# Performance work log

Hardware: AMD Instinct MI355X
Metric: run time of the kernel (lower is better)

The kernel has to match this reference:

```python
import jax, jax.numpy as jnp
import numpy as np

BETA = 0.01  # soft-threshold level (init kwarg)
EPS = 1e-12


def vector_to_toeplitz(v):
    # v: [2N-1] complex generator; T[i, j] = v[N-1 + i - j], shape [N, N]
    n = (v.shape[0] + 1) // 2
    ii = jnp.arange(n)[:, None]
    jj = jnp.arange(n)[None, :]
    return v[(n - 1) + ii - jj]


def soft_thresh(z, beta):
    # complex soft-threshold (proximal op of beta*||.||_1):
    # z * max(|z| - beta, 0) / |z|
    mag = jnp.abs(z)
    scale = jnp.maximum(mag - beta, 0.0) / jnp.maximum(mag, EPS)
    return z * scale.astype(z.real.dtype)


def setup_inputs() -> dict:
    key = jax.random.key(0)
    ks = jax.random.split(key, 8)
    N, M, B = 1024, 256, 1024
    d = jnp.float32
    return {
        "v_re": jax.random.normal(ks[0], (2 * N - 1,), d),
        "v_im": jax.random.normal(ks[1], (2 * N - 1,), d),
        "W2_re": jax.random.normal(ks[2], (N, M), d) / np.sqrt(M),
        "W2_im": jax.random.normal(ks[3], (N, M), d) / np.sqrt(M),
        "x_re": jax.random.normal(ks[4], (N, B), d),
        "x_im": jax.random.normal(ks[5], (N, B), d),
        "y_re": jax.random.normal(ks[6], (M, B), d),
        "y_im": jax.random.normal(ks[7], (M, B), d),
    }


def reference(v_re, v_im, W2_re, W2_im, x_re, x_im, y_re, y_im):
    v = jax.lax.complex(v_re, v_im)      # [2N-1]
    W2 = jax.lax.complex(W2_re, W2_im)   # [N, M] (= A^H)
    x = jax.lax.complex(x_re, x_im)      # [N, B]
    y = jax.lax.complex(y_re, y_im)      # [M, B]
    W1 = vector_to_toeplitz(v)           # [N, N] Toeplitz
    # tpm(W1, x) + W2 @ y, then complex soft-threshold
    z = soft_thresh(W1 @ x + W2 @ y, BETA)  # [N, B]
    return z
```

## Files before the change

kernel.cpp:

```cpp
#include <hip/hip_runtime.h>
#include <hip/hip_fp16.h>
#include <cstdint>
#include <cstddef>


#define K_DIM 2560
#define BETA_F 0.01f
#define EPS_F  1e-12f

typedef __attribute__((ext_vector_type(8))) _Float16 half8;
typedef __attribute__((ext_vector_type(4))) _Float16 half4;
typedef __attribute__((ext_vector_type(4))) float   floatx4;

__device__ alignas(16) _Float16 g_Ap[1024 * K_DIM];
__device__ alignas(16) _Float16 g_Bt[2048 * K_DIM];

__global__ __launch_bounds__(256) void build_all(
    const float* __restrict__ v_re, const float* __restrict__ v_im,
    const float* __restrict__ W2_re, const float* __restrict__ W2_im,
    const float* __restrict__ x_re, const float* __restrict__ x_im,
    const float* __restrict__ y_re, const float* __restrict__ y_im)
{
    const int bx = blockIdx.x;
    if (bx < 1280) {
        int t = bx * 256 + threadIdx.x;
        int i  = t / 320;
        int c  = t - i * 320;
        int kp = c * 8;
        half8 h;
        if (kp < 1024) {
#pragma unroll
            for (int j = 0; j < 8; ++j) h[j] = (_Float16)v_re[1023 + i - kp - j];
        } else if (kp < 1280) {
            const float* s = W2_re + i * 256 + (kp - 1024);
#pragma unroll
            for (int j = 0; j < 8; ++j) h[j] = (_Float16)s[j];
        } else if (kp < 2304) {
            int k2 = kp - 1280;
#pragma unroll
            for (int j = 0; j < 8; ++j) h[j] = (_Float16)v_im[1023 + i - k2 - j];
        } else {
            const float* s = W2_im + i * 256 + (kp - 2304);
#pragma unroll
            for (int j = 0; j < 8; ++j) h[j] = (_Float16)s[j];
        }
        *reinterpret_cast<half8*>(g_Ap + (size_t)i * K_DIM + kp) = h;
        return;
    }
    __shared__ float lre[32][33];
    __shared__ float lim[32][33];
    int idx = bx - 1280;
    int bk  = idx % 40;
    int by  = idx / 40;
    const float* sre = (bk < 32) ? x_re : y_re;
    const float* sim = (bk < 32) ? x_im : y_im;
    int kb   = (bk < 32) ? bk : (bk - 32);
    int koff = (bk < 32) ? 0 : 1024;
    int k0 = kb * 32;
    int n0 = by * 32;
    int tid = threadIdx.x;
    int tx = tid & 31, ty = tid >> 5;
#pragma unroll
    for (int s = 0; s < 4; ++s) {
        int kk = ty + 8 * s;
        lre[kk][tx] = sre[(size_t)(k0 + kk) * 1024 + n0 + tx];
        lim[kk][tx] = sim[(size_t)(k0 + kk) * 1024 + n0 + tx];
    }
    __syncthreads();
    int lane_n = tid >> 3;
    int kq     = (tid & 7) * 4;
    half4 hre, him, hmim;
#pragma unroll
    for (int j = 0; j < 4; ++j) {
        float re = lre[kq + j][lane_n];
        float im = lim[kq + j][lane_n];
        hre[j]  = (_Float16)re;
        him[j]  = (_Float16)im;
        hmim[j] = (_Float16)(-im);
    }
    int n = n0 + lane_n;
    size_t kk2 = (size_t)koff + k0 + kq;
    _Float16* r0 = g_Bt + (size_t)(2 * n)     * K_DIM;
    _Float16* r1 = g_Bt + (size_t)(2 * n + 1) * K_DIM;
    *reinterpret_cast<half4*>(r0 + kk2)        = hre;
    *reinterpret_cast<half4*>(r0 + kk2 + 1280) = hmim;
    *reinterpret_cast<half4*>(r1 + kk2)        = him;
    *reinterpret_cast<half4*>(r1 + kk2 + 1280) = hre;
}

__global__ __launch_bounds__(256, 2) void gemm_fused(float* __restrict__ out,
                                                     int out_n)
{
    __shared__ __align__(16) _Float16 As[2 * 4 * 64 * 32];
    __shared__ __align__(16) _Float16 Bs[2 * 4 * 64 * 32];

    const int tid  = threadIdx.x;
    const int lane = tid & 63;
    const int w    = tid >> 6;
    const int wm   = w >> 1;
    const int wn   = w & 1;

    const int bid = blockIdx.x;
    const int xcd = bid & 7;
    const int t   = bid >> 3;
    const int mi0 = ((xcd & 1) * 8 + (t & 7)) * 64;
    const int ni0 = ((xcd >> 1) * 8 + (t >> 3)) * 64;

    floatx4 acc[2][2];
#pragma unroll
    for (int a = 0; a < 2; ++a)
#pragma unroll
        for (int b = 0; b < 2; ++b) acc[a][b] = (floatx4)0.0f;

    const int rS = tid >> 2;
    const int jS = tid & 3;
    const int s0 = ((rS & 15) >> 1) & 3;
    char* asW = (char*)As + rS * 64 + ((jS ^ s0) * 16);
    char* bsW = (char*)Bs + rS * 64 + ((jS ^ s0) * 16);
    const _Float16* gA = g_Ap + (size_t)(mi0 + rS) * K_DIM + jS * 8;
    const _Float16* gB = g_Bt + (size_t)(ni0 + rS) * K_DIM + jS * 8;

    const int rowA = lane & 15;
    const int q    = lane >> 4;
    const int coff = (q ^ ((rowA >> 1) & 3)) * 16;

    const int NIT = K_DIM / 128;

    half8 sA[2][4], sB[2][4];

    {
        half8 tA[4], tB[4];
#pragma unroll
        for (int ks = 0; ks < 4; ++ks) {
            tA[ks] = *reinterpret_cast<const half8*>(gA + ks * 32);
            tB[ks] = *reinterpret_cast<const half8*>(gB + ks * 32);
        }
#pragma unroll
        for (int ks = 0; ks < 4; ++ks) {
            sA[1][ks] = *reinterpret_cast<const half8*>(gA + 128 + ks * 32);
            sB[1][ks] = *reinterpret_cast<const half8*>(gB + 128 + ks * 32);
        }
#pragma unroll
        for (int ks = 0; ks < 4; ++ks) {
            *reinterpret_cast<half8*>(asW + ks * 4096) = tA[ks];
            *reinterpret_cast<half8*>(bsW + ks * 4096) = tB[ks];
        }
    }
    __syncthreads();

#pragma unroll 2
    for (int kt = 0; kt < NIT; ++kt) {
        const int cur = kt & 1;
        const int nxt = cur ^ 1;
        if (kt + 2 < NIT) {
            const _Float16* ga = gA + (size_t)(kt + 2) * 128;
            const _Float16* gb = gB + (size_t)(kt + 2) * 128;
#pragma unroll
            for (int ks = 0; ks < 4; ++ks) {
                sA[cur][ks] = *reinterpret_cast<const half8*>(ga + ks * 32);
                sB[cur][ks] = *reinterpret_cast<const half8*>(gb + ks * 32);
            }
        }
        const char* Ab = (const char*)As + cur * 16384;
        const char* Bb = (const char*)Bs + cur * 16384;
#pragma unroll
        for (int ks = 0; ks < 4; ++ks) {
            half8 af[2], bf[2];
#pragma unroll
            for (int mi = 0; mi < 2; ++mi) {
                int r = wm * 32 + mi * 16 + rowA;
                af[mi] = *reinterpret_cast<const half8*>(Ab + ks * 4096 + r * 64 + coff);
            }
#pragma unroll
            for (int ni = 0; ni < 2; ++ni) {
                int r = wn * 32 + ni * 16 + rowA;
                bf[ni] = *reinterpret_cast<const half8*>(Bb + ks * 4096 + r * 64 + coff);
            }
#pragma unroll
            for (int mi = 0; mi < 2; ++mi)
#pragma unroll
                for (int ni = 0; ni < 2; ++ni)
                    acc[mi][ni] = __builtin_amdgcn_mfma_f32_16x16x32_f16(
                        af[mi], bf[ni], acc[mi][ni], 0, 0, 0);
        }
        if (kt + 1 < NIT) {
            char* aw = asW + nxt * 16384;
            char* bw = bsW + nxt * 16384;
#pragma unroll
            for (int ks = 0; ks < 4; ++ks) {
                *reinterpret_cast<half8*>(aw + ks * 4096) = sA[nxt][ks];
                *reinterpret_cast<half8*>(bw + ks * 4096) = sB[nxt][ks];
            }
        }
        __syncthreads();
    }

    const int colL  = lane & 15;
    const int rquad = (lane >> 4) * 4;
#pragma unroll
    for (int mi = 0; mi < 2; ++mi)
#pragma unroll
        for (int ni = 0; ni < 2; ++ni)
#pragma unroll
            for (int r = 0; r < 4; ++r) {
                float c = acc[mi][ni][r];
                float p = __shfl_xor(c, 1, 64);
                float mag = sqrtf(c * c + p * p);
                float s = fmaxf(mag - BETA_F, 0.0f) / fmaxf(mag, EPS_F);
                int row = mi0 + wm * 32 + mi * 16 + rquad + r;
                int col = ni0 + wn * 32 + ni * 16 + colL;
                if ((col & 1) == 0) {
                    size_t idx = (size_t)row * 1024 + (col >> 1);
                    if (idx < (size_t)out_n) out[idx] = c * s;
                }
            }
}

extern "C" void kernel_launch(void* const* d_in, const int* in_sizes, int n_in,
                              void* d_out, int out_size, void* d_ws, size_t ws_size,
                              hipStream_t stream) {
    (void)d_ws; (void)ws_size; (void)in_sizes; (void)n_in;
    const float* v_re  = (const float*)d_in[0];
    const float* v_im  = (const float*)d_in[1];
    const float* W2_re = (const float*)d_in[2];
    const float* W2_im = (const float*)d_in[3];
    const float* x_re  = (const float*)d_in[4];
    const float* x_im  = (const float*)d_in[5];
    const float* y_re  = (const float*)d_in[6];
    const float* y_im  = (const float*)d_in[7];
    float* out = (float*)d_out;

    build_all<<<2560, 256, 0, stream>>>(v_re, v_im, W2_re, W2_im,
                                        x_re, x_im, y_re, y_im);
    gemm_fused<<<512, 256, 0, stream>>>(out, out_size);
}
```

Baseline: 107.3 us.

## Merge pack and GEMM kernels into one cooperative kernel with grid sync

Merges the fp16 packing kernel and the fused GEMM+soft-threshold kernel into a single cooperative launch of 512 blocks. Each block packs five virtual pack blocks, then all blocks meet at a grid-wide barrier before the GEMM phase. The aim is to remove the second launch and the gap between the two kernels. In exchange it adds grid-sync overhead, needs all 512 blocks to be co-resident, and the pack phase now runs on fewer blocks and shares the GEMM kernel's resource limits.

```diff
diff --git a/kernel.cpp b/kernel.cpp
--- a/kernel.cpp
+++ b/kernel.cpp
@@ -1,5 +1,6 @@
 #include <hip/hip_runtime.h>
 #include <hip/hip_fp16.h>
+#include <hip/hip_cooperative_groups.h>
 #include <cstdint>
 #include <cstddef>
 
@@ -15,92 +16,96 @@
 __device__ alignas(16) _Float16 g_Ap[1024 * K_DIM];
 __device__ alignas(16) _Float16 g_Bt[2048 * K_DIM];
 
-__global__ __launch_bounds__(256) void build_all(
+namespace cg = cooperative_groups;
+
+__global__ __launch_bounds__(256, 2) void mega(
     const float* __restrict__ v_re, const float* __restrict__ v_im,
     const float* __restrict__ W2_re, const float* __restrict__ W2_im,
     const float* __restrict__ x_re, const float* __restrict__ x_im,
-    const float* __restrict__ y_re, const float* __restrict__ y_im)
-{
-    const int bx = blockIdx.x;
-    if (bx < 1280) {
-        int t = bx * 256 + threadIdx.x;
-        int i  = t / 320;
-        int c  = t - i * 320;
-        int kp = c * 8;
-        half8 h;
-        if (kp < 1024) {
-#pragma unroll
-            for (int j = 0; j < 8; ++j) h[j] = (_Float16)v_re[1023 + i - kp - j];
-        } else if (kp < 1280) {
-            const float* s = W2_re + i * 256 + (kp - 1024);
-#pragma unroll
-            for (int j = 0; j < 8; ++j) h[j] = (_Float16)s[j];
-        } else if (kp < 2304) {
-            int k2 = kp - 1280;
-#pragma unroll
-            for (int j = 0; j < 8; ++j) h[j] = (_Float16)v_im[1023 + i - k2 - j];
-        } else {
-            const float* s = W2_im + i * 256 + (kp - 2304);
-#pragma unroll
-            for (int j = 0; j < 8; ++j) h[j] = (_Float16)s[j];
-        }
-        *reinterpret_cast<half8*>(g_Ap + (size_t)i * K_DIM + kp) = h;
-        return;
-    }
-    __shared__ float lre[32][33];
-    __shared__ float lim[32][33];
-    int idx = bx - 1280;
-    int bk  = idx % 40;
-    int by  = idx / 40;
-    const float* sre = (bk < 32) ? x_re : y_re;
-    const float* sim = (bk < 32) ? x_im : y_im;
-    int kb   = (bk < 32) ? bk : (bk - 32);
-    int koff = (bk < 32) ? 0 : 1024;
-    int k0 = kb * 32;
-    int n0 = by * 32;
-    int tid = threadIdx.x;
-    int tx = tid & 31, ty = tid >> 5;
-#pragma unroll
-    for (int s = 0; s < 4; ++s) {
-        int kk = ty + 8 * s;
-        lre[kk][tx] = sre[(size_t)(k0 + kk) * 1024 + n0 + tx];
-        lim[kk][tx] = sim[(size_t)(k0 + kk) * 1024 + n0 + tx];
-    }
-    __syncthreads();
-    int lane_n = tid >> 3;
-    int kq     = (tid & 7) * 4;
-    half4 hre, him, hmim;
-#pragma unroll
-    for (int j = 0; j < 4; ++j) {
-        float re = lre[kq + j][lane_n];
-        float im = lim[kq + j][lane_n];
-        hre[j]  = (_Float16)re;
-        him[j]  = (_Float16)im;
-        hmim[j] = (_Float16)(-im);
-    }
-    int n = n0 + lane_n;
-    size_t kk2 = (size_t)koff + k0 + kq;
-    _Float16* r0 = g_Bt + (size_t)(2 * n)     * K_DIM;
-    _Float16* r1 = g_Bt + (size_t)(2 * n + 1) * K_DIM;
-    *reinterpret_cast<half4*>(r0 + kk2)        = hre;
-    *reinterpret_cast<half4*>(r0 + kk2 + 1280) = hmim;
-    *reinterpret_cast<half4*>(r1 + kk2)        = him;
-    *reinterpret_cast<half4*>(r1 + kk2 + 1280) = hre;
-}
-
-__global__ __launch_bounds__(256, 2) void gemm_fused(float* __restrict__ out,
-                                                     int out_n)
+    const float* __restrict__ y_re, const float* __restrict__ y_im,
+    float* __restrict__ out, int out_n)
 {
     __shared__ __align__(16) _Float16 As[2 * 4 * 64 * 32];
     __shared__ __align__(16) _Float16 Bs[2 * 4 * 64 * 32];
-
-    const int tid  = threadIdx.x;
+    __shared__ float lre[32][33];
+    __shared__ float lim[32][33];
+
+    const int tid = threadIdx.x;
+    const int bid = blockIdx.x;
+
+    for (int r = 0; r < 5; ++r) {
+        const int vb = bid + 512 * r;
+        if (vb < 1280) {
+            int t = vb * 256 + tid;
+            int i  = t / 320;
+            int c  = t - i * 320;
+            int kp = c * 8;
+            half8 h;
+            if (kp < 1024) {
+#pragma unroll
+                for (int j = 0; j < 8; ++j) h[j] = (_Float16)v_re[1023 + i - kp - j];
+            } else if (kp < 1280) {
+                const float* s = W2_re + i * 256 + (kp - 1024);
+#pragma unroll
+                for (int j = 0; j < 8; ++j) h[j] = (_Float16)s[j];
+            } else if (kp < 2304) {
+                int k2 = kp - 1280;
+#pragma unroll
+                for (int j = 0; j < 8; ++j) h[j] = (_Float16)v_im[1023 + i - k2 - j];
+            } else {
+                const float* s = W2_im + i * 256 + (kp - 2304);
+#pragma unroll
+                for (int j = 0; j < 8; ++j) h[j] = (_Float16)s[j];
+            }
+            *reinterpret_cast<half8*>(g_Ap + (size_t)i * K_DIM + kp) = h;
+        } else {
+            int idx = vb - 1280;
+            int bk  = idx % 40;
+            int by  = idx / 40;
+            const float* sre = (bk < 32) ? x_re : y_re;
+            const float* sim = (bk < 32) ? x_im : y_im;
+            int kb   = (bk < 32) ? bk : (bk - 32);
+            int koff = (bk < 32) ? 0 : 1024;
+            int k0 = kb * 32;
+            int n0 = by * 32;
+            int tx = tid & 31, ty = tid >> 5;
+#pragma unroll
+            for (int s = 0; s < 4; ++s) {
+                int kk = ty + 8 * s;
+                lre[kk][tx] = sre[(size_t)(k0 + kk) * 1024 + n0 + tx];
+                lim[kk][tx] = sim[(size_t)(k0 + kk) * 1024 + n0 + tx];
+            }
+            __syncthreads();
+            int lane_n = tid >> 3;
+            int kq     = (tid & 7) * 4;
+            half4 hre, him, hmim;
+#pragma unroll
+            for (int j = 0; j < 4; ++j) {
+                float re = lre[kq + j][lane_n];
+                float im = lim[kq + j][lane_n];
+                hre[j]  = (_Float16)re;
+                him[j]  = (_Float16)im;
+                hmim[j] = (_Float16)(-im);
+            }
+            int n = n0 + lane_n;
+            size_t kk2 = (size_t)koff + k0 + kq;
+            _Float16* r0 = g_Bt + (size_t)(2 * n)     * K_DIM;
+            _Float16* r1 = g_Bt + (size_t)(2 * n + 1) * K_DIM;
+            *reinterpret_cast<half4*>(r0 + kk2)        = hre;
+            *reinterpret_cast<half4*>(r0 + kk2 + 1280) = hmim;
+            *reinterpret_cast<half4*>(r1 + kk2)        = him;
+            *reinterpret_cast<half4*>(r1 + kk2 + 1280) = hre;
+        }
+        __syncthreads();
+    }
+
+    cg::this_grid().sync();
+
     const int lane = tid & 63;
     const int w    = tid >> 6;
     const int wm   = w >> 1;
     const int wn   = w & 1;
 
-    const int bid = blockIdx.x;
     const int xcd = bid & 7;
     const int t   = bid >> 3;
     const int mi0 = ((xcd & 1) * 8 + (t & 7)) * 64;
@@ -125,7 +130,6 @@
     const int coff = (q ^ ((rowA >> 1) & 3)) * 16;
 
     const int NIT = K_DIM / 128;
-
     half8 sA[2][4], sB[2][4];
 
     {
@@ -168,13 +172,13 @@
             half8 af[2], bf[2];
 #pragma unroll
             for (int mi = 0; mi < 2; ++mi) {
-                int r = wm * 32 + mi * 16 + rowA;
-                af[mi] = *reinterpret_cast<const half8*>(Ab + ks * 4096 + r * 64 + coff);
+                int rr = wm * 32 + mi * 16 + rowA;
+                af[mi] = *reinterpret_cast<const half8*>(Ab + ks * 4096 + rr * 64 + coff);
             }
 #pragma unroll
             for (int ni = 0; ni < 2; ++ni) {
-                int r = wn * 32 + ni * 16 + rowA;
-                bf[ni] = *reinterpret_cast<const half8*>(Bb + ks * 4096 + r * 64 + coff);
+                int rr = wn * 32 + ni * 16 + rowA;
+                bf[ni] = *reinterpret_cast<const half8*>(Bb + ks * 4096 + rr * 64 + coff);
             }
 #pragma unroll
             for (int mi = 0; mi < 2; ++mi)
@@ -202,12 +206,12 @@
 #pragma unroll
         for (int ni = 0; ni < 2; ++ni)
 #pragma unroll
-            for (int r = 0; r < 4; ++r) {
-                float c = acc[mi][ni][r];
+            for (int rr = 0; rr < 4; ++rr) {
+                float c = acc[mi][ni][rr];
                 float p = __shfl_xor(c, 1, 64);
                 float mag = sqrtf(c * c + p * p);
                 float s = fmaxf(mag - BETA_F, 0.0f) / fmaxf(mag, EPS_F);
-                int row = mi0 + wm * 32 + mi * 16 + rquad + r;
+                int row = mi0 + wm * 32 + mi * 16 + rquad + rr;
                 int col = ni0 + wn * 32 + ni * 16 + colL;
                 if ((col & 1) == 0) {
                     size_t idx = (size_t)row * 1024 + (col >> 1);
@@ -229,8 +233,10 @@
     const float* y_re  = (const float*)d_in[6];
     const float* y_im  = (const float*)d_in[7];
     float* out = (float*)d_out;
-
-    build_all<<<2560, 256, 0, stream>>>(v_re, v_im, W2_re, W2_im,
-                                        x_re, x_im, y_re, y_im);
-    gemm_fused<<<512, 256, 0, stream>>>(out, out_size);
+    int out_n = out_size;
+
+    void* args[] = { &v_re, &v_im, &W2_re, &W2_im,
+                     &x_re, &x_im, &y_re, &y_im, &out, &out_n };
+    hipLaunchCooperativeKernel((void*)mega, dim3(512), dim3(256),
+                               args, 0, stream);
 }
```

Measured after the change: 200.2 us. 1.87x slower.

## Store compact re/im B planes and synthesize negated block in GEMM loader

Applied to the files above, without the earlier changes.

The build kernel no longer writes the 2x-expanded real-embedded B matrix with a duplicated and negated block. It writes only two compact fp16 planes (re and im). The GEMM loader picks the right plane per row parity and K-half, and flips sign bits when storing to LDS. This halves the B workspace written and cut by the prep kernel, at the cost of extra address logic and XOR ops in the GEMM loop. B global reads in the GEMM stay the same size but now hit a smaller, more cache-friendly footprint.

```diff
diff --git a/kernel.cpp b/kernel.cpp
--- a/kernel.cpp
+++ b/kernel.cpp
@@ -5,6 +5,7 @@
 
 
 #define K_DIM 2560
+#define BPLANE (1024 * 1280)
 #define BETA_F 0.01f
 #define EPS_F  1e-12f
 
@@ -13,7 +14,15 @@
 typedef __attribute__((ext_vector_type(4))) float   floatx4;
 
 __device__ alignas(16) _Float16 g_Ap[1024 * K_DIM];
-__device__ alignas(16) _Float16 g_Bt[2048 * K_DIM];
+__device__ alignas(16) _Float16 g_Bc[2 * BPLANE];
+
+__device__ __forceinline__ half8 negh8(half8 v, bool neg) {
+    if (!neg) return v;
+    union { half8 h; unsigned u[4]; } t; t.h = v;
+#pragma unroll
+    for (int i = 0; i < 4; ++i) t.u[i] ^= 0x80008000u;
+    return t.h;
+}
 
 __global__ __launch_bounds__(256) void build_all(
     const float* __restrict__ v_re, const float* __restrict__ v_im,
@@ -69,23 +78,16 @@
     __syncthreads();
     int lane_n = tid >> 3;
     int kq     = (tid & 7) * 4;
-    half4 hre, him, hmim;
+    half4 hre, him;
 #pragma unroll
     for (int j = 0; j < 4; ++j) {
-        float re = lre[kq + j][lane_n];
-        float im = lim[kq + j][lane_n];
-        hre[j]  = (_Float16)re;
-        him[j]  = (_Float16)im;
-        hmim[j] = (_Float16)(-im);
+        hre[j] = (_Float16)lre[kq + j][lane_n];
+        him[j] = (_Float16)lim[kq + j][lane_n];
     }
     int n = n0 + lane_n;
-    size_t kk2 = (size_t)koff + k0 + kq;
-    _Float16* r0 = g_Bt + (size_t)(2 * n)     * K_DIM;
-    _Float16* r1 = g_Bt + (size_t)(2 * n + 1) * K_DIM;
-    *reinterpret_cast<half4*>(r0 + kk2)        = hre;
-    *reinterpret_cast<half4*>(r0 + kk2 + 1280) = hmim;
-    *reinterpret_cast<half4*>(r1 + kk2)        = him;
-    *reinterpret_cast<half4*>(r1 + kk2 + 1280) = hre;
+    size_t kk2 = (size_t)n * 1280 + koff + k0 + kq;
+    *reinterpret_cast<half4*>(g_Bc + kk2)          = hre;
+    *reinterpret_cast<half4*>(g_Bc + BPLANE + kk2) = him;
 }
 
 __global__ __launch_bounds__(256, 2) void gemm_fused(float* __restrict__ out,
@@ -118,7 +120,8 @@
     char* asW = (char*)As + rS * 64 + ((jS ^ s0) * 16);
     char* bsW = (char*)Bs + rS * 64 + ((jS ^ s0) * 16);
     const _Float16* gA = g_Ap + (size_t)(mi0 + rS) * K_DIM + jS * 8;
-    const _Float16* gB = g_Bt + (size_t)(ni0 + rS) * K_DIM + jS * 8;
+    const size_t bRow  = (size_t)(ni0 / 2 + (rS >> 1)) * 1280 + jS * 8;
+    const int    rpar  = rS & 1;
 
     const int rowA = lane & 15;
     const int q    = lane >> 4;
@@ -126,19 +129,27 @@
 
     const int NIT = K_DIM / 128;
 
+    auto gbSlab = [&](int sl) -> const _Float16* {
+        int hf = (sl >= 10);
+        return g_Bc + (size_t)(rpar ^ hf) * BPLANE + bRow
+                    + (size_t)sl * 128 - (size_t)hf * 1280;
+    };
+
     half8 sA[2][4], sB[2][4];
 
     {
+        const _Float16* gb0 = gbSlab(0);
+        const _Float16* gb1 = gbSlab(1);
         half8 tA[4], tB[4];
 #pragma unroll
         for (int ks = 0; ks < 4; ++ks) {
             tA[ks] = *reinterpret_cast<const half8*>(gA + ks * 32);
-            tB[ks] = *reinterpret_cast<const half8*>(gB + ks * 32);
+            tB[ks] = *reinterpret_cast<const half8*>(gb0 + ks * 32);
         }
 #pragma unroll
         for (int ks = 0; ks < 4; ++ks) {
             sA[1][ks] = *reinterpret_cast<const half8*>(gA + 128 + ks * 32);
-            sB[1][ks] = *reinterpret_cast<const half8*>(gB + 128 + ks * 32);
+            sB[1][ks] = *reinterpret_cast<const half8*>(gb1 + ks * 32);
         }
 #pragma unroll
         for (int ks = 0; ks < 4; ++ks) {
@@ -154,7 +165,7 @@
         const int nxt = cur ^ 1;
         if (kt + 2 < NIT) {
             const _Float16* ga = gA + (size_t)(kt + 2) * 128;
-            const _Float16* gb = gB + (size_t)(kt + 2) * 128;
+            const _Float16* gb = gbSlab(kt + 2);
 #pragma unroll
             for (int ks = 0; ks < 4; ++ks) {
                 sA[cur][ks] = *reinterpret_cast<const half8*>(ga + ks * 32);
@@ -184,12 +195,13 @@
                         af[mi], bf[ni], acc[mi][ni], 0, 0, 0);
         }
         if (kt + 1 < NIT) {
+            const bool neg = ((kt + 1) >= 10) && (rpar == 0);
             char* aw = asW + nxt * 16384;
             char* bw = bsW + nxt * 16384;
 #pragma unroll
             for (int ks = 0; ks < 4; ++ks) {
                 *reinterpret_cast<half8*>(aw + ks * 4096) = sA[nxt][ks];
-                *reinterpret_cast<half8*>(bw + ks * 4096) = sB[nxt][ks];
+                *reinterpret_cast<half8*>(bw + ks * 4096) = negh8(sB[nxt][ks], neg);
             }
         }
         __syncthreads();
```

After: 109.1 us. About the same (+1.7%).
